# Kernel optimization log

Hardware: AMD Instinct MI355X
Metric: run time of the kernel (lower is better)

The kernel has to match this reference:

```python
import jax, jax.numpy as jnp
import numpy as np

B, L, D = 4, 512, 2880          # packed sequences, tokens per seq, hidden
N, K, H = 64, 8, 64             # query heads, kv heads, head dim
G = N // K                      # GQA group size
WINDOW = 128                    # sliding window (gpt-oss window layer)
SM_SCALE = 1.0 / H ** 0.5
THETA = 150000.0
INIT_CTX = 4096.0
SCALING = 32.0
NTK_ALPHA = 1.0
NTK_BETA = 32.0
NEG = -1e30


def _rope_tables(positions):
    # GPT-OSS YaRN NTK-by-parts rotary tables.
    d_half = H // 2
    freq = THETA ** (jnp.arange(0, H, 2, dtype=jnp.float32) / H)
    concentration = 0.1 * np.log(SCALING) + 1.0
    low = d_half * np.log(INIT_CTX / (NTK_BETA * 2 * np.pi)) / np.log(THETA)
    high = d_half * np.log(INIT_CTX / (NTK_ALPHA * 2 * np.pi)) / np.log(THETA)
    interp = 1.0 / (SCALING * freq)
    extrap = 1.0 / freq
    ramp = jnp.clip((jnp.arange(d_half, dtype=jnp.float32) - low) / (high - low), 0.0, 1.0)
    blend = 1.0 - ramp
    inv_freq = interp * (1.0 - blend) + extrap * blend
    ang = positions.astype(jnp.float32)[:, None] * inv_freq[None, :]  # [T, H/2]
    return jnp.cos(ang) * concentration, jnp.sin(ang) * concentration


def _apply_rope(x, cos, sin):
    # x: [T, heads, H]; half-split rotation as in gpt-oss.
    x1, x2 = x[..., : H // 2], x[..., H // 2:]
    c, s = cos[:, None, :], sin[:, None, :]
    return jnp.concatenate([x1 * c - x2 * s, x2 * c + x1 * s], axis=-1)


def setup_inputs() -> dict:
    key = jax.random.key(0)
    ks = jax.random.split(key, 10)
    T = B * L
    return {
        "x": jax.random.normal(ks[0], (T, D), jnp.float32),
        "wq": jax.random.normal(ks[1], (D, N, H), jnp.float32) * 0.02,
        "bq": jax.random.normal(ks[2], (N, H), jnp.float32) * 0.02,
        "wk": jax.random.normal(ks[3], (D, K, H), jnp.float32) * 0.02,
        "bk": jax.random.normal(ks[4], (K, H), jnp.float32) * 0.02,
        "wv": jax.random.normal(ks[5], (D, K, H), jnp.float32) * 0.02,
        "bv": jax.random.normal(ks[6], (K, H), jnp.float32) * 0.02,
        "wo": jax.random.normal(ks[7], (N, H, D), jnp.float32) * 0.02,
        "bo": jax.random.normal(ks[8], (D,), jnp.float32) * 0.02,
        "sinks": jax.random.normal(ks[9], (N,), jnp.float32),
        "positions": jnp.tile(jnp.arange(L, dtype=jnp.int32), B),  # per-seq positions
    }


def reference(x, wq, bq, wk, bk, wv, bv, wo, bo, sinks, positions):
    # fused QKV projections
    q = jnp.einsum('td,dnh->tnh', x, wq) + bq            # [T,N,H]
    k = jnp.einsum('td,dkh->tkh', x, wk) + bk            # [T,K,H]
    v = jnp.einsum('td,dkh->tkh', x, wv) + bv            # [T,K,H]
    cos, sin = _rope_tables(positions)
    q = _apply_rope(q, cos, sin)
    k = _apply_rope(k, cos, sin)
    # unpack ragged tokens into [B, L, ...] (equal-length packed sequences)
    qb = q.reshape(B, L, K, G, H)
    kb = k.reshape(B, L, K, H)
    vb = v.reshape(B, L, K, H)
    s = jnp.einsum('blkgh,bmkh->bkglm', qb, kb) * SM_SCALE  # [B,K,G,L,L]
    pos = jnp.arange(L)
    delta = pos[:, None] - pos[None, :]
    allowed = (delta >= 0) & (delta < WINDOW)               # causal + sliding window
    s = jnp.where(allowed, s, NEG)
    # attention sinks: extra per-head logit joining the softmax denominator only
    sink = sinks.reshape(K, G)[None, :, :, None]            # [1,K,G,1]
    m = jnp.maximum(jnp.max(s, axis=-1), sink)              # [B,K,G,L]
    p = jnp.exp(s - m[..., None])
    denom = jnp.exp(sink - m) + jnp.sum(p, axis=-1)         # [B,K,G,L]
    o = jnp.einsum('bkglm,bmkh->blkgh', p, vb)
    o = o / jnp.transpose(denom, (0, 3, 1, 2))[..., None]   # [B,L,K,G,H]
    attn = o.reshape(B * L, N, H)
    return jnp.einsum('tnh,nhd->td', attn, wo) + bo         # [T,D]
```

## Files before the change

kernel.cpp:

```cpp
#include <hip/hip_runtime.h>
#include <hip/hip_bf16.h>

#define TB 4
#define TL 512
#define TD 2880
#define TN 64
#define TKH 8
#define TH 64
#define TG 8
#define TWIN 128
#define TT (TB*TL)

typedef unsigned short u16;
typedef __attribute__((ext_vector_type(8))) short bf16x8;
typedef __attribute__((ext_vector_type(4))) float f32x4;

__device__ __forceinline__ u16 f2b(float f) {
  unsigned u = __float_as_uint(f);
  u += 0x7fffu + ((u >> 16) & 1u);
  return (u16)(u >> 16);
}
__device__ __forceinline__ float b2f(u16 u) {
  return __uint_as_float(((unsigned)u) << 16);
}

__device__ __forceinline__ void load_lds16(const u16* g, u16* l) {
  __builtin_amdgcn_global_load_lds(
      (const __attribute__((address_space(1))) unsigned int*)g,
      (__attribute__((address_space(3))) unsigned int*)l, 16, 0, 0);
}

template<int BN, int ROPE>
__global__ __launch_bounds__(256, 4) void gemm_sn(
    const u16* __restrict__ A, const u16* __restrict__ Bt,
    const float* __restrict__ bias, void* __restrict__ Cv,
    const int* __restrict__ positions,
    int Kd, int Nc, int ldc, int out_bf16, int nx)
{
  constexpr int NF = BN / 32;
  __shared__ u16 As[128*64];
  __shared__ u16 Bs[BN*64];

  const int tid  = threadIdx.x;
  const int lane = tid & 63;
  const int wave = tid >> 6;

  int id = blockIdx.x;
  const int cpx = gridDim.x >> 3;
  id = (id & 7)*cpx + (id >> 3);
  const int rgsz = nx << 3;
  const int rg   = id / rgsz;
  const int rem  = id - rg*rgsz;
  const int bm = (rg*8 + (rem & 7)) * 128;
  const int bn = (rem >> 3) * BN;

  const int wr = (wave >> 1) * 64;
  const int wc = ROPE ? (wave & 1) * 16 : (wave & 1) * (BN/2);
  constexpr int NSTR = ROPE ? 32 : 16;

  f32x4 acc[4][NF];
#pragma unroll
  for (int i = 0; i < 4; ++i)
#pragma unroll
    for (int j = 0; j < NF; ++j) acc[i][j] = (f32x4){0.f,0.f,0.f,0.f};

  const int rr   = tid >> 3;
  const int sseg = (tid & 7) ^ (rr & 7);
  const u16* aS = A  + (size_t)(bm + rr)*Kd + sseg*8;
  const u16* bS = Bt + (size_t)(bn + rr)*Kd + sseg*8;

  const int fr = lane & 15, kq = lane >> 4;
  const int swz = lane & 7;

  const int NT = Kd >> 6;
  for (int t = 0; t < NT; ++t) {
    const int k0 = t << 6;
#pragma unroll
    for (int i = 0; i < 4; ++i)
      load_lds16(aS + (size_t)i*32*Kd + k0, &As[i*2048 + wave*512]);
#pragma unroll
    for (int i = 0; i < BN/32; ++i)
      load_lds16(bS + (size_t)i*32*Kd + k0, &Bs[i*2048 + wave*512]);
    __syncthreads();

#pragma unroll
    for (int s = 0; s < 2; ++s) {
      const int ch = ((s*4 + kq) ^ swz) * 16;
      bf16x8 af[4], bv[NF];
#pragma unroll
      for (int mi = 0; mi < 4; ++mi) {
        const int row = wr + mi*16 + fr;
        af[mi] = *(const bf16x8*)((const char*)&As[row*64] + ch);
      }
#pragma unroll
      for (int ni = 0; ni < NF; ++ni) {
        const int row = wc + ni*NSTR + fr;
        bv[ni] = *(const bf16x8*)((const char*)&Bs[row*64] + ch);
      }
#pragma unroll
      for (int mi = 0; mi < 4; ++mi)
#pragma unroll
        for (int ni = 0; ni < NF; ++ni)
          acc[mi][ni] = __builtin_amdgcn_mfma_f32_16x16x32_bf16(
              af[mi], bv[ni], acc[mi][ni], 0, 0, 0);
    }
    __syncthreads();
  }

  const int rbase = bm + wr + (lane >> 4)*4;

  if (ROPE) {
    constexpr int NP = NF / 2;
    const int i = wc + (lane & 15);
    const float lnth = 11.918390573078392f;
    const float low  = 8.092779f;
    const float high = 17.398025f;
    const float conc = 1.3465735903f;
    const float fi = (float)i * 0.03125f;
    const float itp = __expf(-fi * lnth);
    float ramp = ((float)i - low) * (1.0f/(high - low));
    ramp = fminf(fmaxf(ramp, 0.0f), 1.0f);
    const float invf = itp*(1.0f/32.0f)*ramp + itp*(1.0f - ramp);

    u16* Cb = (u16*)Cv;
#pragma unroll
    for (int p = 0; p < NP; ++p) {
      const int hb = bn + p*64;
      const int col1 = hb + i, col2 = col1 + 32;
      const int htype = (hb < 4096) ? 0 : (hb < 4608 ? 1 : 2);
      const float mul = (htype == 0) ? (conc * 0.125f) : conc;
      const float b1 = bias[col1], b2 = bias[col2];
#pragma unroll
      for (int mi = 0; mi < 4; ++mi) {
#pragma unroll
        for (int j = 0; j < 4; ++j) {
          const int row = rbase + mi*16 + j;
          float x1 = acc[mi][2*p+0][j] + b1;
          float x2 = acc[mi][2*p+1][j] + b2;
          if (htype < 2) {
            const float ang = (float)positions[row] * invf;
            const float cc = cosf(ang) * mul;
            const float ss = sinf(ang) * mul;
            const float y1 = x1*cc - x2*ss;
            const float y2 = x2*cc + x1*ss;
            x1 = y1; x2 = y2;
          }
          Cb[(size_t)row*ldc + col1] = f2b(x1);
          Cb[(size_t)row*ldc + col2] = f2b(x2);
        }
      }
    }
  } else {
    const int cbase = bn + wc + (lane & 15);
#pragma unroll
    for (int mi = 0; mi < 4; ++mi) {
#pragma unroll
      for (int ni = 0; ni < NF; ++ni) {
        const int col = cbase + ni*NSTR;
        const float bvl = (col < Nc) ? bias[col] : 0.f;
#pragma unroll
        for (int j = 0; j < 4; ++j) {
          const int row = rbase + mi*16 + j;
          const float val = acc[mi][ni][j] + bvl;
          if (out_bf16) {
            ((u16*)Cv)[(size_t)row*ldc + col] = f2b(val);
          } else if (col < Nc) {
            ((float*)Cv)[(size_t)row*ldc + col] = val;
          }
        }
      }
    }
  }
}

__device__ __forceinline__ void tconv_into(
    float (*tile)[33], const float* __restrict__ in, u16* __restrict__ out,
    int R, int C, int bx, int by, int tid)
{
  const int c0 = bx*32, r0 = by*32;
  const int tx = tid & 31, ty = tid >> 5;
#pragma unroll
  for (int i = 0; i < 4; ++i)
    tile[ty + i*8][tx] = in[(size_t)(r0 + ty + i*8)*C + c0 + tx];
  __syncthreads();
#pragma unroll
  for (int i = 0; i < 4; ++i) {
    const int oc = ty + i*8;
    out[(size_t)(c0 + oc)*R + r0 + tx] = f2b(tile[tx][oc]);
  }
}

__global__ __launch_bounds__(256) void prep_kernel(
    const float* __restrict__ x,  const float* __restrict__ wq,
    const float* __restrict__ wk, const float* __restrict__ wv,
    const float* __restrict__ wo, const float* __restrict__ bq,
    const float* __restrict__ bk, const float* __restrict__ bv,
    u16* __restrict__ xb, u16* __restrict__ wqkvt, u16* __restrict__ wot,
    float* __restrict__ bqkv)
{
  __shared__ float tile[32][33];
  const int b = blockIdx.x;
  const int tid = threadIdx.x;

  if (b < 5760) {
    const int i = b*256 + tid;
    float4 f = ((const float4*)x)[i];
    ushort4 o;
    o.x = f2b(f.x); o.y = f2b(f.y); o.z = f2b(f.z); o.w = f2b(f.w);
    ((ushort4*)xb)[i] = o;
  } else if (b < 17280) {
    const int local = b - 5760;
    tconv_into(tile, wq, wqkvt, TD, 4096, local % 128, local / 128, tid);
  } else if (b < 18720) {
    const int local = b - 17280;
    tconv_into(tile, wk, wqkvt + (size_t)4096*TD, TD, 512,
               local % 16, local / 16, tid);
  } else if (b < 20160) {
    const int local = b - 18720;
    tconv_into(tile, wv, wqkvt + (size_t)4608*TD, TD, 512,
               local % 16, local / 16, tid);
  } else if (b < 31680) {
    const int local = b - 20160;
    tconv_into(tile, wo, wot, 4096, TD, local % 90, local / 90, tid);
  } else if (b < 31936) {
    const int i = (b - 31680)*256 + tid;
    ((ushort4*)(wot + (size_t)2880*4096))[i] = (ushort4){0,0,0,0};
  } else {
    const int i = (b - 31936)*256 + tid;
    if (i < 5120)
      bqkv[i] = (i < 4096) ? bq[i] : (i < 4608 ? bk[i-4096] : bv[i-4608]);
  }
}

__global__ __launch_bounds__(512) void attn3_kernel(
    const u16* __restrict__ qkv, u16* __restrict__ obuf,
    const float* __restrict__ sinks)
{
  __shared__ u16 Kl[192*64];
  __shared__ u16 Vt[64*192];
  __shared__ u16 Pl[8][2048];

  const int lt = blockIdx.x, kh = blockIdx.y, b = blockIdx.z;
  const int l0 = lt*64;
  const int mstart = (l0 > 127) ? (l0 - 127) : 0;
  const int mcnt = l0 + 64 - mstart;
  const int NC = (mcnt + 31) >> 5;
  const int base = l0 - mstart;

  const int tid = threadIdx.x;
  const int lane = tid & 63;
  const int g = tid >> 6;
  const int lL = lane & 15;
  const int q = lane >> 4;

  {
    const u16* kv0 = qkv + ((size_t)(b*TL + mstart)*5120 + 4096 + kh*64);
    for (int s = tid; s < 1536; s += 512) {
      const int m = s >> 3, hs = s & 7;
      uint4 kx = make_uint4(0,0,0,0), vx = make_uint4(0,0,0,0);
      if (m < mcnt) {
        const u16* gp = kv0 + (size_t)m*5120 + hs*8;
        kx = *(const uint4*)gp;
        vx = *(const uint4*)(gp + 512);
      }
      *(uint4*)((char*)&Kl[m*64] + ((hs*16) ^ ((m&7)<<4))) = kx;
      const unsigned vw[4] = {vx.x, vx.y, vx.z, vx.w};
#pragma unroll
      for (int i = 0; i < 8; ++i) {
        const int h = hs*8 + i;
        const u16 val = (u16)(vw[i>>1] >> ((i&1)*16));
        *(u16*)((char*)&Vt[h*192] + ((m*2) ^ (((h>>3)&7)<<4))) = val;
      }
    }
  }

  bf16x8 qb[4][2];
  {
    const u16* qbase = qkv + ((size_t)(b*TL + l0)*5120 + (kh*8 + g)*64);
#pragma unroll
    for (int l4 = 0; l4 < 4; ++l4)
#pragma unroll
      for (int kk = 0; kk < 2; ++kk)
        qb[l4][kk] = *(const bf16x8*)(qbase + (size_t)(l4*16 + lL)*5120 + kk*32 + q*8);
  }
  const float sink = sinks[kh*8 + g];
  __syncthreads();

  float Mrun[4] = {-1e30f,-1e30f,-1e30f,-1e30f};
  float Dden[4] = {0.f,0.f,0.f,0.f};
  f32x4 oacc[4][4];
#pragma unroll
  for (int i = 0; i < 4; ++i)
#pragma unroll
    for (int j = 0; j < 4; ++j) oacc[i][j] = (f32x4){0.f,0.f,0.f,0.f};

  u16* Pw = &Pl[g][0];

  for (int c = 0; c < NC; ++c) {
    bf16x8 ka[2][2];
#pragma unroll
    for (int m2 = 0; m2 < 2; ++m2) {
      const int row = c*32 + m2*16 + lL;
#pragma unroll
      for (int kk = 0; kk < 2; ++kk)
        ka[m2][kk] = *(const bf16x8*)((char*)&Kl[row*64] +
                       ((kk*64 + q*16) ^ ((row&7)<<4)));
    }
    bf16x8 vb[4];
#pragma unroll
    for (int hf = 0; hf < 4; ++hf) {
      const int h = hf*16 + lL;
      vb[hf] = *(const bf16x8*)((char*)&Vt[h*192] +
                 ((c*64 + q*16) ^ (((h>>3)&7)<<4)));
    }

#pragma unroll
    for (int l4 = 0; l4 < 4; ++l4) {
      const int lo = base + l4*16;
      if (c*32 > lo + 15 || c*32 + 31 < lo - 127) continue;

      const f32x4 z = (f32x4){0.f,0.f,0.f,0.f};
      f32x4 s0 = __builtin_amdgcn_mfma_f32_16x16x32_bf16(ka[0][0], qb[l4][0], z, 0,0,0);
      s0 = __builtin_amdgcn_mfma_f32_16x16x32_bf16(ka[0][1], qb[l4][1], s0, 0,0,0);
      f32x4 s1 = __builtin_amdgcn_mfma_f32_16x16x32_bf16(ka[1][0], qb[l4][0], z, 0,0,0);
      s1 = __builtin_amdgcn_mfma_f32_16x16x32_bf16(ka[1][1], qb[l4][1], s1, 0,0,0);

      float sv[2][4];
      bool  al[2][4];
      float cmax = -1e30f;
#pragma unroll
      for (int m2 = 0; m2 < 2; ++m2)
#pragma unroll
        for (int j = 0; j < 4; ++j) {
          const int delta = (lo + lL) - (c*32 + m2*16 + q*4 + j);
          const bool a = (delta >= 0) && (delta < TWIN);
          const float s = (m2 ? s1[j] : s0[j]);
          sv[m2][j] = s;
          al[m2][j] = a;
          if (a) cmax = fmaxf(cmax, s);
        }
      cmax = fmaxf(cmax, __shfl_xor(cmax, 16));
      cmax = fmaxf(cmax, __shfl_xor(cmax, 32));
      const float Mn = fmaxf(Mrun[l4], cmax);
      const float r = __expf(Mrun[l4] - Mn);
      Mrun[l4] = Mn;

      float ls = 0.f;
      u16 pb[2][4];
#pragma unroll
      for (int m2 = 0; m2 < 2; ++m2)
#pragma unroll
        for (int j = 0; j < 4; ++j) {
          const float p = al[m2][j] ? __expf(sv[m2][j] - Mn) : 0.f;
          ls += p;
          pb[m2][j] = f2b(p);
        }
      ls += __shfl_xor(ls, 16);
      ls += __shfl_xor(ls, 32);
      Dden[l4] = Dden[l4]*r + ls;

      const int l = l4*16 + lL;
#pragma unroll
      for (int m2 = 0; m2 < 2; ++m2) {
        uint2 w;
        w.x = (unsigned)pb[m2][0] | ((unsigned)pb[m2][1] << 16);
        w.y = (unsigned)pb[m2][2] | ((unsigned)pb[m2][3] << 16);
        *(uint2*)((char*)Pw + l*64 + ((m2*32 + q*8) ^ ((l&3)<<4))) = w;
      }

      float rb[4];
#pragma unroll
      for (int j = 0; j < 4; ++j) rb[j] = __shfl(r, q*4 + j);
#pragma unroll
      for (int hf = 0; hf < 4; ++hf)
#pragma unroll
        for (int j = 0; j < 4; ++j) oacc[l4][hf][j] *= rb[j];

      bf16x8 pa = *(const bf16x8*)((char*)Pw + l*64 + ((q*16) ^ ((l&3)<<4)));
#pragma unroll
      for (int hf = 0; hf < 4; ++hf)
        oacc[l4][hf] = __builtin_amdgcn_mfma_f32_16x16x32_bf16(
            pa, vb[hf], oacc[l4][hf], 0, 0, 0);
    }
  }

#pragma unroll
  for (int l4 = 0; l4 < 4; ++l4) {
    const float di = 1.0f / (Dden[l4] + __expf(sink - Mrun[l4]));
    float db[4];
#pragma unroll
    for (int j = 0; j < 4; ++j) db[j] = __shfl(di, q*4 + j);
#pragma unroll
    for (int hf = 0; hf < 4; ++hf)
#pragma unroll
      for (int j = 0; j < 4; ++j) {
        const int row = l0 + l4*16 + q*4 + j;
        obuf[(size_t)(b*TL + row)*4096 + (kh*8 + g)*64 + hf*16 + lL] =
            f2b(oacc[l4][hf][j] * db[j]);
      }
  }
}

extern "C" void kernel_launch(void* const* d_in, const int* in_sizes, int n_in,
                              void* d_out, int out_size, void* d_ws, size_t ws_size,
                              hipStream_t stream)
{
  const float* x     = (const float*)d_in[0];
  const float* wq    = (const float*)d_in[1];
  const float* bq    = (const float*)d_in[2];
  const float* wk    = (const float*)d_in[3];
  const float* bk    = (const float*)d_in[4];
  const float* wv    = (const float*)d_in[5];
  const float* bv    = (const float*)d_in[6];
  const float* wo    = (const float*)d_in[7];
  const float* bo    = (const float*)d_in[8];
  const float* sinks = (const float*)d_in[9];
  const int* positions = (const int*)d_in[10];
  float* out = (float*)d_out;

  u16* xb    = (u16*)d_ws;
  u16* wqkvt = xb + (size_t)TT*TD;
  u16* wot   = wqkvt + (size_t)5120*TD;
  u16* qkv   = wot + (size_t)2944*4096;
  u16* obuf  = qkv + (size_t)TT*5120;
  float* bqkv = (float*)(obuf + (size_t)TT*4096);

  prep_kernel<<<31956, 256, 0, stream>>>(
      x, wq, wk, wv, wo, bq, bk, bv, xb, wqkvt, wot, bqkv);

  gemm_sn<128, 1><<<640, 256, 0, stream>>>(
      xb, wqkvt, bqkv, qkv, positions, TD, 5120, 5120, 1, 40);

  attn3_kernel<<<dim3(8, TKH, TB), 512, 0, stream>>>(qkv, obuf, sinks);

  gemm_sn<64, 0><<<720, 256, 0, stream>>>(
      obuf, wot, bo, out, nullptr, 4096, 2880, 2880, 0, 45);
}
```

Measured before the change: 192.2 us.

## Double-buffer LDS tiles in GEMM and widen output-projection tile to 128

The GEMM now uses two LDS buffers per operand. The next K-tile's global_load_lds is issued before computing on the current one, with an explicit vmcnt wait and raw barriers in place of the two __syncthreads per iteration. MFMA sections are wrapped in s_setprio to favour compute issue. The output projection switches from BN=64 with 720 blocks to BN=128 with 368 blocks, which covers 2944 columns against 2880 real ones. The doubled LDS and lower launch-bounds occupancy (4 to 2) trade latency hiding by other blocks for intra-block overlap. The wider output tile relies on the epilogue guarding columns past Nc.

```diff
diff --git a/kernel.cpp b/kernel.cpp
--- a/kernel.cpp
+++ b/kernel.cpp
@@ -31,15 +31,16 @@
 }
 
 template<int BN, int ROPE>
-__global__ __launch_bounds__(256, 4) void gemm_sn(
+__global__ __launch_bounds__(256, 2) void gemm_db2(
     const u16* __restrict__ A, const u16* __restrict__ Bt,
     const float* __restrict__ bias, void* __restrict__ Cv,
     const int* __restrict__ positions,
     int Kd, int Nc, int ldc, int out_bf16, int nx)
 {
+  static_assert(BN == 128, "vmcnt(8) literal assumes 8 loads/thread/tile");
   constexpr int NF = BN / 32;
-  __shared__ u16 As[128*64];
-  __shared__ u16 Bs[BN*64];
+  __shared__ u16 As[2][128*64];
+  __shared__ u16 Bs[2][BN*64];
 
   const int tid  = threadIdx.x;
   const int lane = tid & 63;
@@ -69,19 +70,32 @@
   const u16* aS = A  + (size_t)(bm + rr)*Kd + sseg*8;
   const u16* bS = Bt + (size_t)(bn + rr)*Kd + sseg*8;
 
+#define STG(dc, kt) do {                                             \
+    const int _k0 = (kt) << 6;                                       \
+    _Pragma("unroll")                                                \
+    for (int _i = 0; _i < 4; ++_i)                                   \
+      load_lds16(aS + (size_t)_i*32*Kd + _k0, &As[dc][_i*2048 + wave*512]); \
+    _Pragma("unroll")                                                \
+    for (int _i = 0; _i < 4; ++_i)                                   \
+      load_lds16(bS + (size_t)_i*32*Kd + _k0, &Bs[dc][_i*2048 + wave*512]); \
+  } while (0)
+
   const int fr = lane & 15, kq = lane >> 4;
   const int swz = lane & 7;
 
   const int NT = Kd >> 6;
+  STG(0, 0);
+
   for (int t = 0; t < NT; ++t) {
-    const int k0 = t << 6;
-#pragma unroll
-    for (int i = 0; i < 4; ++i)
-      load_lds16(aS + (size_t)i*32*Kd + k0, &As[i*2048 + wave*512]);
-#pragma unroll
-    for (int i = 0; i < BN/32; ++i)
-      load_lds16(bS + (size_t)i*32*Kd + k0, &Bs[i*2048 + wave*512]);
-    __syncthreads();
+    const int c = t & 1;
+    if (t + 1 < NT) {
+      STG(c ^ 1, t + 1);
+      asm volatile("s_waitcnt vmcnt(8)" ::: "memory");
+    } else {
+      asm volatile("s_waitcnt vmcnt(0)" ::: "memory");
+    }
+    __builtin_amdgcn_s_barrier();
+    __builtin_amdgcn_sched_barrier(0);
 
 #pragma unroll
     for (int s = 0; s < 2; ++s) {
@@ -90,22 +104,27 @@
 #pragma unroll
       for (int mi = 0; mi < 4; ++mi) {
         const int row = wr + mi*16 + fr;
-        af[mi] = *(const bf16x8*)((const char*)&As[row*64] + ch);
+        af[mi] = *(const bf16x8*)((const char*)&As[c][row*64] + ch);
       }
 #pragma unroll
       for (int ni = 0; ni < NF; ++ni) {
         const int row = wc + ni*NSTR + fr;
-        bv[ni] = *(const bf16x8*)((const char*)&Bs[row*64] + ch);
-      }
+        bv[ni] = *(const bf16x8*)((const char*)&Bs[c][row*64] + ch);
+      }
+      __builtin_amdgcn_s_setprio(1);
 #pragma unroll
       for (int mi = 0; mi < 4; ++mi)
 #pragma unroll
         for (int ni = 0; ni < NF; ++ni)
           acc[mi][ni] = __builtin_amdgcn_mfma_f32_16x16x32_bf16(
               af[mi], bv[ni], acc[mi][ni], 0, 0, 0);
-    }
-    __syncthreads();
-  }
+      __builtin_amdgcn_s_setprio(0);
+    }
+
+    __builtin_amdgcn_s_barrier();
+    __builtin_amdgcn_sched_barrier(0);
+  }
+#undef STG
 
   const int rbase = bm + wr + (lane >> 4)*4;
 
@@ -428,11 +447,11 @@
   prep_kernel<<<31956, 256, 0, stream>>>(
       x, wq, wk, wv, wo, bq, bk, bv, xb, wqkvt, wot, bqkv);
 
-  gemm_sn<128, 1><<<640, 256, 0, stream>>>(
+  gemm_db2<128, 1><<<640, 256, 0, stream>>>(
       xb, wqkvt, bqkv, qkv, positions, TD, 5120, 5120, 1, 40);
 
   attn3_kernel<<<dim3(8, TKH, TB), 512, 0, stream>>>(qkv, obuf, sinks);
 
-  gemm_sn<64, 0><<<720, 256, 0, stream>>>(
-      obuf, wot, bo, out, nullptr, 4096, 2880, 2880, 0, 45);
-}
+  gemm_db2<128, 0><<<368, 256, 0, stream>>>(
+      obuf, wot, bo, out, nullptr, 4096, 2880, 2880, 0, 23);
+}
```

Result: slower. 252.4 us (+31.3%).
